# Optimization experiments

Measured on AMD Instinct MI355X. Metric: run time of the kernel, lower is better.

The kernel has to match this reference:

```python
import jax, jax.numpy as jnp
import numpy as np

D = 4096  # must be a power of 2


def fwht(x):
    """Unnormalized fast Walsh-Hadamard transform along the last axis.

    log2(d)-stage butterfly; the Python while loop is over a static, small
    number of stages (12 for d=4096), each stage fully vectorized.
    """
    orig_shape = x.shape
    d = orig_shape[-1]
    x = x.reshape(-1, d)
    h = 1
    while h < d:
        # group into (rows, d//(2h), 2, h) butterflies
        x = x.reshape(-1, d // (2 * h), 2, h)
        a = x[:, :, 0, :]
        b = x[:, :, 1, :]
        x = jnp.stack([a + b, a - b], axis=2).reshape(-1, d)
        h *= 2
    return x.reshape(orig_shape)


def setup_inputs() -> dict:
    key = jax.random.key(0)
    kx, ks = jax.random.split(key)
    x = jax.random.normal(kx, (4, 4096, D), dtype=jnp.float32)
    # sign buffer: random +/-1 per coordinate ('tbq' pattern -> pseudo-random signs)
    signs = jnp.where(jax.random.bernoulli(ks, 0.5, (D,)), 1.0, -1.0).astype(jnp.float32)
    return {"x": x, "signs": signs}


def reference(x, signs):
    # x_rot = H(x * S): elementwise sign flip, then unnormalized FWHT
    return fwht(x * signs)
```

## Files before the change

### kernel.cpp

```cpp
#include <hip/hip_runtime.h>

#define FWHT_D 4096

typedef float v4f __attribute__((ext_vector_type(4)));

static __device__ __forceinline__ int swz(int i) {
    return i ^ (((i >> 6) & 7) << 2);
}

static __device__ __forceinline__ void bfly(float& a, float& b) {
    float s = a + b;
    float d = a - b;
    a = s; b = d;
}

__global__ __launch_bounds__(256, 2) void fwht_kernel(const float* __restrict__ x,
                                                      const float* __restrict__ signs,
                                                      float* __restrict__ out) {
    __shared__ float lds[FWHT_D];

    const int row = blockIdx.x;
    const int t   = threadIdx.x;
    const float* xr  = x   + (size_t)row * FWHT_D;
    float*       orw = out + (size_t)row * FWHT_D;

    float r[4][4];
#pragma unroll
    for (int k = 0; k < 4; ++k) {
        const int i = 1024 * k + 4 * t;
        v4f xv = __builtin_nontemporal_load((const v4f*)(xr + i));
        v4f sv = *(const v4f*)(signs + i);
        v4f p  = xv * sv;
        r[k][0] = p.x; r[k][1] = p.y; r[k][2] = p.z; r[k][3] = p.w;
    }
#pragma unroll
    for (int k = 0; k < 4; ++k) {
        bfly(r[k][0], r[k][1]);
        bfly(r[k][2], r[k][3]);
        bfly(r[k][0], r[k][2]);
        bfly(r[k][1], r[k][3]);
    }
#pragma unroll
    for (int pass = 0; pass < 2; ++pass) {
        const int b = 1 << pass;
#pragma unroll
        for (int k = 0; k < 4; ++k) {
            if (!(k & b)) {
#pragma unroll
                for (int e = 0; e < 4; ++e)
                    bfly(r[k][e], r[k | b][e]);
            }
        }
    }
#pragma unroll
    for (int k = 0; k < 4; ++k) {
        const int i = 1024 * k + 4 * t;
        v4f p = { r[k][0], r[k][1], r[k][2], r[k][3] };
        *(v4f*)&lds[swz(i)] = p;
    }
    __syncthreads();

    {
        const int B = t >> 2;
        const int c = t & 3;
        const int s = B & 7;
        float v[16];
#pragma unroll
        for (int j = 0; j < 16; ++j)
            v[j] = lds[(B * 64 + 4 * j + c) ^ (s << 2)];

#pragma unroll
        for (int pass = 0; pass < 4; ++pass) {
            const int b = 1 << pass;
#pragma unroll
            for (int j = 0; j < 16; ++j)
                if (!(j & b)) bfly(v[j], v[j | b]);
        }

#pragma unroll
        for (int j = 0; j < 16; ++j)
            lds[(B * 64 + 4 * j + c) ^ (s << 2)] = v[j];
    }
    __syncthreads();

    {
        const int w = t >> 6;
        const int l = t & 63;
        float v[16];
#pragma unroll
        for (int j = 0; j < 16; ++j)
            v[j] = lds[(1024 * w + 64 * j + l) ^ ((j & 7) << 2)];

#pragma unroll
        for (int pass = 0; pass < 4; ++pass) {
            const int b = 1 << pass;
#pragma unroll
            for (int j = 0; j < 16; ++j)
                if (!(j & b)) bfly(v[j], v[j | b]);
        }

#pragma unroll
        for (int j = 0; j < 16; ++j)
            __builtin_nontemporal_store(v[j], orw + 1024 * w + 64 * j + l);
    }
}

extern "C" void kernel_launch(void* const* d_in, const int* in_sizes, int n_in,
                              void* d_out, int out_size, void* d_ws, size_t ws_size,
                              hipStream_t stream) {
    const float* x     = (const float*)d_in[0];
    const float* signs = (const float*)d_in[1];
    float* out = (float*)d_out;

    const int rows = in_sizes[0] / FWHT_D;
    dim3 grid(rows), block(256);
    fwht_kernel<<<grid, block, 0, stream>>>(x, signs, out);
}
```

Before: 91.56 us.

## Process each row with a single 64-lane wave holding 64 values per lane

The kernel now uses one 64-thread wavefront per row instead of 256 threads. Each lane keeps 64 elements in registers, so the transform needs only two register-resident stages around one LDS transpose instead of three. The final output is read back through LDS and written as vectorized 16-byte stores. The cost is much higher register pressure and only 64 threads per block, which can cut occupancy and the ability to hide memory latency in a bandwidth-bound kernel.

```diff
diff --git a/kernel.cpp b/kernel.cpp
--- a/kernel.cpp
+++ b/kernel.cpp
@@ -5,7 +5,7 @@
 typedef float v4f __attribute__((ext_vector_type(4)));
 
 static __device__ __forceinline__ int swz(int i) {
-    return i ^ (((i >> 6) & 7) << 2);
+    return i ^ (((i >> 8) & 7) << 2);
 }
 
 static __device__ __forceinline__ void bfly(float& a, float& b) {
@@ -14,94 +14,82 @@
     a = s; b = d;
 }
 
-__global__ __launch_bounds__(256, 2) void fwht_kernel(const float* __restrict__ x,
-                                                      const float* __restrict__ signs,
-                                                      float* __restrict__ out) {
+__global__ __launch_bounds__(64, 2) void fwht_kernel(const float* __restrict__ x,
+                                                     const float* __restrict__ signs,
+                                                     float* __restrict__ out) {
     __shared__ float lds[FWHT_D];
 
     const int row = blockIdx.x;
-    const int t   = threadIdx.x;
+    const int L   = threadIdx.x;
     const float* xr  = x   + (size_t)row * FWHT_D;
     float*       orw = out + (size_t)row * FWHT_D;
 
-    float r[4][4];
+    float v[64];
+
 #pragma unroll
-    for (int k = 0; k < 4; ++k) {
-        const int i = 1024 * k + 4 * t;
-        v4f xv = __builtin_nontemporal_load((const v4f*)(xr + i));
-        v4f sv = *(const v4f*)(signs + i);
-        v4f p  = xv * sv;
-        r[k][0] = p.x; r[k][1] = p.y; r[k][2] = p.z; r[k][3] = p.w;
+    for (int q = 0; q < 16; ++q) {
+        v4f xv = __builtin_nontemporal_load((const v4f*)(xr + q * 256 + 4 * L));
+        v[4 * q + 0] = xv.x; v[4 * q + 1] = xv.y;
+        v[4 * q + 2] = xv.z; v[4 * q + 3] = xv.w;
     }
 #pragma unroll
-    for (int k = 0; k < 4; ++k) {
-        bfly(r[k][0], r[k][1]);
-        bfly(r[k][2], r[k][3]);
-        bfly(r[k][0], r[k][2]);
-        bfly(r[k][1], r[k][3]);
+    for (int q = 0; q < 16; ++q) {
+        v4f sv = *(const v4f*)(signs + q * 256 + 4 * L);
+        v[4 * q + 0] *= sv.x; v[4 * q + 1] *= sv.y;
+        v[4 * q + 2] *= sv.z; v[4 * q + 3] *= sv.w;
+    }
+
+#pragma unroll
+    for (int q = 0; q < 16; ++q) {
+        bfly(v[4 * q + 0], v[4 * q + 1]);
+        bfly(v[4 * q + 2], v[4 * q + 3]);
+        bfly(v[4 * q + 0], v[4 * q + 2]);
+        bfly(v[4 * q + 1], v[4 * q + 3]);
     }
 #pragma unroll
-    for (int pass = 0; pass < 2; ++pass) {
+    for (int pass = 0; pass < 4; ++pass) {
         const int b = 1 << pass;
 #pragma unroll
-        for (int k = 0; k < 4; ++k) {
-            if (!(k & b)) {
+        for (int q = 0; q < 16; ++q) {
+            if (!(q & b)) {
 #pragma unroll
                 for (int e = 0; e < 4; ++e)
-                    bfly(r[k][e], r[k | b][e]);
+                    bfly(v[4 * q + e], v[4 * (q | b) + e]);
             }
         }
     }
+
 #pragma unroll
-    for (int k = 0; k < 4; ++k) {
-        const int i = 1024 * k + 4 * t;
-        v4f p = { r[k][0], r[k][1], r[k][2], r[k][3] };
-        *(v4f*)&lds[swz(i)] = p;
+    for (int q = 0; q < 16; ++q) {
+        v4f p = { v[4 * q + 0], v[4 * q + 1], v[4 * q + 2], v[4 * q + 3] };
+        *(v4f*)&lds[(q * 256 + 4 * L) ^ ((q & 7) << 2)] = p;
     }
     __syncthreads();
 
-    {
-        const int B = t >> 2;
-        const int c = t & 3;
-        const int s = B & 7;
-        float v[16];
+    const int hi = (L >> 2) * 256 + (L & 3);
+    const int sx = ((L >> 2) & 7) << 2;
 #pragma unroll
-        for (int j = 0; j < 16; ++j)
-            v[j] = lds[(B * 64 + 4 * j + c) ^ (s << 2)];
+    for (int j = 0; j < 64; ++j)
+        v[j] = lds[(hi + 4 * j) ^ sx];
 
 #pragma unroll
-        for (int pass = 0; pass < 4; ++pass) {
-            const int b = 1 << pass;
+    for (int pass = 0; pass < 6; ++pass) {
+        const int b = 1 << pass;
 #pragma unroll
-            for (int j = 0; j < 16; ++j)
-                if (!(j & b)) bfly(v[j], v[j | b]);
-        }
-
-#pragma unroll
-        for (int j = 0; j < 16; ++j)
-            lds[(B * 64 + 4 * j + c) ^ (s << 2)] = v[j];
+        for (int j = 0; j < 64; ++j)
+            if (!(j & b)) bfly(v[j], v[j | b]);
     }
     __syncthreads();
 
-    {
-        const int w = t >> 6;
-        const int l = t & 63;
-        float v[16];
 #pragma unroll
-        for (int j = 0; j < 16; ++j)
-            v[j] = lds[(1024 * w + 64 * j + l) ^ ((j & 7) << 2)];
+    for (int j = 0; j < 64; ++j)
+        lds[(hi + 4 * j) ^ sx] = v[j];
+    __syncthreads();
 
 #pragma unroll
-        for (int pass = 0; pass < 4; ++pass) {
-            const int b = 1 << pass;
-#pragma unroll
-            for (int j = 0; j < 16; ++j)
-                if (!(j & b)) bfly(v[j], v[j | b]);
-        }
-
-#pragma unroll
-        for (int j = 0; j < 16; ++j)
-            __builtin_nontemporal_store(v[j], orw + 1024 * w + 64 * j + l);
+    for (int m = 0; m < 16; ++m) {
+        v4f p = *(const v4f*)&lds[(m * 256 + 4 * L) ^ ((m & 7) << 2)];
+        __builtin_nontemporal_store(p, (v4f*)(orw + m * 256 + 4 * L));
     }
 }
 
@@ -113,6 +101,6 @@
     float* out = (float*)d_out;
 
     const int rows = in_sizes[0] / FWHT_D;
-    dim3 grid(rows), block(256);
+    dim3 grid(rows), block(64);
     fwht_kernel<<<grid, block, 0, stream>>>(x, signs, out);
 }
```

Result: slower. 94.35 us (+3.0%).
